# Performance work log

Measured on AMD Instinct MI355X. Metric: run time of the kernel, lower is better.

Reference implementation:

```python
import jax, jax.numpy as jnp
import numpy as np

N = 50000        # nodes
E = 1_600_000    # edges
F_IN = 128
HID = 128
OUT = 128
NEG_SLOPE = 0.2  # PyG GATConv default


def _gat_layer(x, src, dst, W, a_src, a_dst, b, n_nodes):
    """PyG GATConv (heads=1, add_self_loops handled by caller)."""
    h = x @ W                                   # [N, d_out]
    alpha_src = h @ a_src                       # [N]
    alpha_dst = h @ a_dst                       # [N]
    e = jax.nn.leaky_relu(alpha_src[src] + alpha_dst[dst], NEG_SLOPE)  # [E']
    # segment softmax over incoming edges of each destination node
    m = jax.ops.segment_max(e, dst, num_segments=n_nodes)
    e = jnp.exp(e - m[dst])
    s = jax.ops.segment_sum(e, dst, num_segments=n_nodes)
    alpha = e / s[dst]                          # [E']
    out = jax.ops.segment_sum(alpha[:, None] * h[src], dst, num_segments=n_nodes)
    return out + b


def setup_inputs() -> dict:
    key = jax.random.key(0)
    ks = jax.random.split(key, 11)
    sW1 = 1.0 / np.sqrt(F_IN)
    sW2 = 1.0 / np.sqrt(HID)
    return {
        "x": jax.random.normal(ks[0], (N, F_IN), dtype=jnp.float32),
        "edge_index": jax.random.randint(ks[1], (2, E), 0, N, dtype=jnp.int64
                                         if jax.config.jax_enable_x64 else jnp.int32),
        "W1": jax.random.normal(ks[2], (F_IN, HID), dtype=jnp.float32) * sW1,
        "a1_src": jax.random.normal(ks[3], (HID,), dtype=jnp.float32) * sW2,
        "a1_dst": jax.random.normal(ks[4], (HID,), dtype=jnp.float32) * sW2,
        "b1": jnp.zeros((HID,), dtype=jnp.float32),
        "W2": jax.random.normal(ks[5], (HID, OUT), dtype=jnp.float32) * sW2,
        "a2_src": jax.random.normal(ks[6], (OUT,), dtype=jnp.float32) * sW2,
        "a2_dst": jax.random.normal(ks[7], (OUT,), dtype=jnp.float32) * sW2,
        "b2": jnp.zeros((OUT,), dtype=jnp.float32),
    }


def reference(x, edge_index, W1, a1_src, a1_dst, b1, W2, a2_src, a2_dst, b2):
    n = x.shape[0]
    loop = jnp.arange(n, dtype=edge_index.dtype)
    src = jnp.concatenate([edge_index[0], loop])   # add self loops (PyG default)
    dst = jnp.concatenate([edge_index[1], loop])
    h = _gat_layer(x, src, dst, W1, a1_src, a1_dst, b1, n)
    h = jax.nn.relu(h)
    # F.dropout with training=False is identity (eval-mode reference)
    out = _gat_layer(h, src, dst, W2, a2_src, a2_dst, b2, n)
    return out
```

## Files before the change

kernel.cpp:

```cpp
#include <hip/hip_runtime.h>
#include <hip/hip_bf16.h>
#include <hip/hip_fp16.h>

#define FD 128
#define CBW 256
#define NBK 256

typedef _Float16 half8 __attribute__((ext_vector_type(8)));
typedef float f32x4 __attribute__((ext_vector_type(4)));

__global__ __launch_bounds__(256) void k_pre(const int* __restrict__ dst,
                                             int* __restrict__ ccnt, int e, int nb,
                                             const float* __restrict__ W1,
                                             const float* __restrict__ W2,
                                             __half* __restrict__ T1,
                                             __half* __restrict__ T2) {
    __shared__ float sw[128 * 129];
    const int t = threadIdx.x;
    if (blockIdx.x < 256) {
        int* lh = (int*)sw;
        if (t < NBK) lh[t] = 0;
        __syncthreads();
        for (int i = blockIdx.x * 256 + t; i < e; i += 256 * 256)
            atomicAdd(&lh[dst[i] >> 8], 1);
        __syncthreads();
        if (t < nb) {
            int c = lh[t];
            if (c) atomicAdd(&ccnt[t], c);
        }
    } else {
        const float* W = (blockIdx.x == 257) ? W2 : W1;
        __half* T = (blockIdx.x == 257) ? T2 : T1;
#pragma unroll
        for (int i = 0; i < 64; i++) {
            int idx = i * 256 + t;
            sw[(idx >> 7) * 129 + (idx & 127)] = W[idx];
        }
        __syncthreads();
#pragma unroll
        for (int i = 0; i < 32; i++) {
            int o = i * 256 + t;
            int c = o >> 6, kp = o & 63;
            float lo = sw[(kp * 2) * 129 + c];
            float hi = sw[(kp * 2 + 1) * 129 + c];
            *(__half2*)&T[c * 128 + kp * 2] = __floats2half2_rn(lo, hi);
        }
    }
}

__global__ void k_cscan(const int* __restrict__ ccnt, int* __restrict__ cbase,
                        int* __restrict__ ccur, int nb, int* __restrict__ rowptr, int n) {
    __shared__ int wsum[16];
    __shared__ int woff[17];
    const int t = threadIdx.x, lane = t & 63, wid = t >> 6;
    int v = (t < nb) ? ccnt[t] : 0;
    int s = v;
#pragma unroll
    for (int off = 1; off < 64; off <<= 1) {
        int u = __shfl_up(s, off, 64);
        if (lane >= off) s += u;
    }
    if (lane == 63) wsum[wid] = s;
    __syncthreads();
    if (wid == 0) {
        int w2 = (lane < 16) ? wsum[lane] : 0;
#pragma unroll
        for (int off = 1; off < 16; off <<= 1) {
            int u = __shfl_up(w2, off, 64);
            if (lane >= off) w2 += u;
        }
        if (lane < 16) woff[lane + 1] = w2;
        if (lane == 0) woff[0] = 0;
    }
    __syncthreads();
    int excl = woff[wid] + (s - v);
    if (t < nb) { cbase[t] = excl; ccur[t] = excl; }
    if (t == 0) { cbase[nb] = woff[16]; rowptr[n] = woff[16]; }
}

__global__ __launch_bounds__(256) void k_mid(const int* __restrict__ src,
                                             const int* __restrict__ dst,
                                             int* __restrict__ ccur,
                                             int* __restrict__ ebuf,
                                             int e, int nb, int nscat,
                                             const float* __restrict__ X,
                                             const __half* __restrict__ Wt,
                                             const float* __restrict__ a_s,
                                             const float* __restrict__ a_d,
                                             __half* __restrict__ H,
                                             float* __restrict__ as_,
                                             float* __restrict__ ad_, int n) {
    __shared__ int lh[NBK];
    __shared__ int lb[NBK];
    const int t = threadIdx.x;
    if ((int)blockIdx.x < nscat) {
        const int per = (e + nscat - 1) / nscat;
        const int lo = blockIdx.x * per;
        const int hi = min(e, lo + per);
        if (t < NBK) lh[t] = 0;
        __syncthreads();
        for (int i = lo + t; i < hi; i += 256) atomicAdd(&lh[dst[i] >> 8], 1);
        __syncthreads();
        if (t < nb) {
            int c = lh[t];
            lb[t] = c ? atomicAdd(&ccur[t], c) : 0;
        }
        __syncthreads();
        if (t < NBK) lh[t] = 0;
        __syncthreads();
        for (int i = lo + t; i < hi; i += 256) {
            int d = dst[i];
            int bkt = d >> 8;
            int r = atomicAdd(&lh[bkt], 1);
            ebuf[lb[bkt] + r] = (src[i] << 8) | (d & (CBW - 1));
        }
    } else {
        const int bid = blockIdx.x - nscat;
        const int wave = t >> 6, lane = t & 63;
        const int g = lane >> 4, c16 = lane & 15;
        const int row0 = bid * 64 + wave * 16;

        half8 A[4];
        {
            int row = row0 + c16;
            int rc = (row < n) ? row : (n - 1);
            const float* xp = &X[(size_t)rc * 128 + g * 8];
#pragma unroll
            for (int kc = 0; kc < 4; kc++) {
                float4 x0 = *(const float4*)(xp + kc * 32);
                float4 x1 = *(const float4*)(xp + kc * 32 + 4);
                half8 a;
                a[0] = (_Float16)x0.x; a[1] = (_Float16)x0.y;
                a[2] = (_Float16)x0.z; a[3] = (_Float16)x0.w;
                a[4] = (_Float16)x1.x; a[5] = (_Float16)x1.y;
                a[6] = (_Float16)x1.z; a[7] = (_Float16)x1.w;
                A[kc] = a;
            }
        }
        f32x4 acc[8];
#pragma unroll
        for (int ct = 0; ct < 8; ct++) acc[ct] = (f32x4){0.f, 0.f, 0.f, 0.f};
#pragma unroll
        for (int ct = 0; ct < 8; ct++) {
            const __half* wp = &Wt[(ct * 16 + c16) * 128 + g * 8];
#pragma unroll
            for (int kc = 0; kc < 4; kc++) {
                half8 b = *(const half8*)(wp + kc * 32);
                acc[ct] = __builtin_amdgcn_mfma_f32_16x16x32_f16(A[kc], b, acc[ct], 0, 0, 0);
            }
        }
        float asv[8], adv[8];
#pragma unroll
        for (int ct = 0; ct < 8; ct++) {
            asv[ct] = a_s[ct * 16 + c16];
            adv[ct] = a_d[ct * 16 + c16];
        }
#pragma unroll
        for (int r = 0; r < 4; r++) {
            const int row = row0 + g * 4 + r;
            float vs = 0.f, vd = 0.f;
#pragma unroll
            for (int ct = 0; ct < 8; ct++) {
                float v = acc[ct][r];
                vs += v * asv[ct];
                vd += v * adv[ct];
                if (row < n) H[(size_t)row * 128 + ct * 16 + c16] = __float2half(v);
            }
#pragma unroll
            for (int off = 8; off; off >>= 1) {
                vs += __shfl_xor(vs, off, 16);
                vd += __shfl_xor(vd, off, 16);
            }
            if (c16 == 0 && row < n) { as_[row] = vs; ad_[row] = vd; }
        }
    }
}

__global__ __launch_bounds__(256) void k_fine(const int* __restrict__ ebuf,
                                              const int* __restrict__ cbase,
                                              int* __restrict__ rowptr,
                                              int* __restrict__ colidx, int n) {
    const int b = blockIdx.x;
    const int node0 = b * CBW;
    const int nloc = min(CBW, n - node0);
    const int beg = cbase[b], end = cbase[b + 1];
    __shared__ int fh[CBW];
    __shared__ int fo[CBW];
    __shared__ int wt4[4];
    const int t = threadIdx.x, lane = t & 63, wid = t >> 6;
    fh[t] = 0;
    __syncthreads();
    for (int e = beg + t; e < end; e += 256) atomicAdd(&fh[ebuf[e] & (CBW - 1)], 1);
    __syncthreads();
    {
        int v = fh[t];
        int s = v;
#pragma unroll
        for (int off = 1; off < 64; off <<= 1) {
            int u = __shfl_up(s, off, 64);
            if (lane >= off) s += u;
        }
        if (lane == 63) wt4[wid] = s;
        __syncthreads();
        int wo = 0;
#pragma unroll
        for (int j = 0; j < 4; j++) wo += (j < wid) ? wt4[j] : 0;
        fo[t] = wo + s - v;
    }
    __syncthreads();
    if (t < nloc) rowptr[node0 + t] = beg + fo[t];
    fh[t] = 0;
    __syncthreads();
    for (int e = beg + t; e < end; e += 256) {
        int v = ebuf[e];
        int d = v & (CBW - 1);
        int r = atomicAdd(&fh[d], 1);
        colidx[beg + fo[d] + r] = v >> 8;
    }
}

__global__ __launch_bounds__(256) void k_gemm(const __half* __restrict__ X,
                                              const __half* __restrict__ Wt,
                                              const float* __restrict__ a_s,
                                              const float* __restrict__ a_d,
                                              __half* __restrict__ H,
                                              float* __restrict__ as_,
                                              float* __restrict__ ad_, int n) {
    const int t = threadIdx.x;
    const int wave = t >> 6, lane = t & 63;
    const int g = lane >> 4, c16 = lane & 15;
    const int row0 = blockIdx.x * 64 + wave * 16;

    half8 A[4];
    {
        int row = row0 + c16;
        int rc = (row < n) ? row : (n - 1);
        const __half* xp = &X[(size_t)rc * 128 + g * 8];
#pragma unroll
        for (int kc = 0; kc < 4; kc++) A[kc] = *(const half8*)(xp + kc * 32);
    }
    f32x4 acc[8];
#pragma unroll
    for (int ct = 0; ct < 8; ct++) acc[ct] = (f32x4){0.f, 0.f, 0.f, 0.f};
#pragma unroll
    for (int ct = 0; ct < 8; ct++) {
        const __half* wp = &Wt[(ct * 16 + c16) * 128 + g * 8];
#pragma unroll
        for (int kc = 0; kc < 4; kc++) {
            half8 b = *(const half8*)(wp + kc * 32);
            acc[ct] = __builtin_amdgcn_mfma_f32_16x16x32_f16(A[kc], b, acc[ct], 0, 0, 0);
        }
    }
    float asv[8], adv[8];
#pragma unroll
    for (int ct = 0; ct < 8; ct++) {
        asv[ct] = a_s[ct * 16 + c16];
        adv[ct] = a_d[ct * 16 + c16];
    }
#pragma unroll
    for (int r = 0; r < 4; r++) {
        const int row = row0 + g * 4 + r;
        float vs = 0.f, vd = 0.f;
#pragma unroll
        for (int ct = 0; ct < 8; ct++) {
            float v = acc[ct][r];
            vs += v * asv[ct];
            vd += v * adv[ct];
            if (row < n) H[(size_t)row * 128 + ct * 16 + c16] = __float2half(v);
        }
#pragma unroll
        for (int off = 8; off; off >>= 1) {
            vs += __shfl_xor(vs, off, 16);
            vd += __shfl_xor(vd, off, 16);
        }
        if (c16 == 0 && row < n) { as_[row] = vs; ad_[row] = vd; }
    }
}

__device__ __forceinline__ void fmix8(float* acc, uint4 hv, float w) {
    union { uint4 u; _Float16 h[8]; } c;
    c.u = hv;
#pragma unroll
    for (int j = 0; j < 8; j++) acc[j] += w * (float)c.h[j];
}

__global__ __launch_bounds__(256) void k_aggr(const __half* __restrict__ H,
                                              const float* __restrict__ as_,
                                              const float* __restrict__ ad_,
                                              const int* __restrict__ rowptr,
                                              const int* __restrict__ colidx,
                                              const float* __restrict__ bias,
                                              float* __restrict__ outf,
                                              __half* __restrict__ outh,
                                              int n, int mode) {
    __shared__ int2 pr[4][64];
    const int wid = threadIdx.x >> 6;
    const int lane = threadIdx.x & 63;
    const int node = blockIdx.x * 4 + wid;
    if (node >= n) return;
    const int q = lane >> 4;
    const int boff = (lane & 15) * 16;
    const char* Hb = (const char*)H + boff;
    const float adn = ad_[node];
    float sp = 0.f;
    float acc[8] = {0.f, 0.f, 0.f, 0.f, 0.f, 0.f, 0.f, 0.f};
    const int beg = rowptr[node], end = rowptr[node + 1];

    {
        float e = as_[node] + adn;
        e = (e > 0.f) ? e : 0.2f * e;
        const float w = __expf(e);
        if (lane == 63) sp += w;
        if (q == 3) {
            const uint4 hv = *(const uint4*)(Hb + ((unsigned)node << 8));
            fmix8(acc, hv, w);
        }
    }

    for (int it = beg; it < end; it += 64) {
        const int idx = it + lane;
        const bool valid = idx < end;
        const int sl = colidx[valid ? idx : (end - 1)];
        float e = as_[sl] + adn;
        e = (e > 0.f) ? e : 0.2f * e;
        const float w = valid ? __expf(e) : 0.f;
        sp += w;
        pr[wid][lane] = make_int2((int)((unsigned)sl << 8), __float_as_int(w));
        int m = end - it; if (m > 64) m = 64;
        const int iters = (m + 3) >> 2;
        int slot = q;
#pragma unroll 4
        for (int g = 0; g < iters; ++g) {
            const int2 p = pr[wid][slot];
            const float wg = __int_as_float(p.y);
            const uint4 hv = *(const uint4*)(Hb + (unsigned)p.x);
            fmix8(acc, hv, wg);
            slot += 4;
        }
    }

#pragma unroll
    for (int off = 1; off < 64; off <<= 1) sp += __shfl_xor(sp, off);
#pragma unroll
    for (int off = 16; off <= 32; off <<= 1) {
#pragma unroll
        for (int j = 0; j < 8; j++) acc[j] += __shfl_xor(acc[j], off);
    }
    if (q == 0) {
        const int f0 = boff >> 1;
        const float inv = 1.f / sp;
        float o[8];
        const float4 b0 = *(const float4*)&bias[f0];
        const float4 b1 = *(const float4*)&bias[f0 + 4];
        o[0] = acc[0] * inv + b0.x; o[1] = acc[1] * inv + b0.y;
        o[2] = acc[2] * inv + b0.z; o[3] = acc[3] * inv + b0.w;
        o[4] = acc[4] * inv + b1.x; o[5] = acc[5] * inv + b1.y;
        o[6] = acc[6] * inv + b1.z; o[7] = acc[7] * inv + b1.w;
        if (mode == 1) {
#pragma unroll
            for (int j = 0; j < 8; j++) o[j] = fmaxf(o[j], 0.f);
            union { __half2 h2[4]; uint4 u; } pkk;
            pkk.h2[0] = __floats2half2_rn(o[0], o[1]);
            pkk.h2[1] = __floats2half2_rn(o[2], o[3]);
            pkk.h2[2] = __floats2half2_rn(o[4], o[5]);
            pkk.h2[3] = __floats2half2_rn(o[6], o[7]);
            *(uint4*)&outh[(size_t)node * 128 + f0] = pkk.u;
        } else {
            *(float4*)&outf[(size_t)node * 128 + f0] = make_float4(o[0], o[1], o[2], o[3]);
            *(float4*)&outf[(size_t)node * 128 + f0 + 4] = make_float4(o[4], o[5], o[6], o[7]);
        }
    }
}

extern "C" void kernel_launch(void* const* d_in, const int* in_sizes, int n_in,
                              void* d_out, int out_size, void* d_ws, size_t ws_size,
                              hipStream_t stream) {
    const float* x   = (const float*)d_in[0];
    const int*   ei  = (const int*)d_in[1];
    const float* W1  = (const float*)d_in[2];
    const float* a1s = (const float*)d_in[3];
    const float* a1d = (const float*)d_in[4];
    const float* b1  = (const float*)d_in[5];
    const float* W2  = (const float*)d_in[6];
    const float* a2s = (const float*)d_in[7];
    const float* a2d = (const float*)d_in[8];
    const float* b2  = (const float*)d_in[9];
    float* dout = (float*)d_out;

    const int n = in_sizes[0] / FD;
    const int E = in_sizes[1] / 2;
    const int* src = ei;
    const int* dst = ei + E;
    const int NB = (n + CBW - 1) / CBW;

    char* base = (char*)d_ws;
    __half* buf0  = (__half*)base;
    int*    ebuf  = (int*)base;
    __half* H     = (__half*)(base + (size_t)n * FD * sizeof(__half));
    float* as_    = (float*)((char*)H + (size_t)n * FD * sizeof(__half));
    float* ad_    = as_ + n;
    int*   rowptr = (int*)(ad_ + n);
    int*   ccnt   = rowptr + (n + 1);
    int*   cbase  = ccnt + NB;
    int*   ccur   = cbase + NB + 1;
    int*   colidx = ccur + NB;
    size_t wt_off = (((size_t)((char*)(colidx + E) - base)) + 15) & ~(size_t)15;
    __half* Wt1h  = (__half*)(base + wt_off);
    __half* Wt2h  = Wt1h + 128 * 128;

    const int gemm_grid = (n + 63) / 64;
    const int node_grid = (n + 3) / 4;
    const int SCAT = 256;

    hipMemsetAsync(ccnt, 0, (size_t)NB * sizeof(int), stream);
    k_pre<<<258, 256, 0, stream>>>(dst, ccnt, E, NB, W1, W2, Wt1h, Wt2h);
    k_cscan<<<1, 1024, 0, stream>>>(ccnt, cbase, ccur, NB, rowptr, n);
    k_mid<<<SCAT + gemm_grid, 256, 0, stream>>>(src, dst, ccur, ebuf, E, NB, SCAT,
                                                x, Wt1h, a1s, a1d, H, as_, ad_, n);
    k_fine<<<NB, 256, 0, stream>>>(ebuf, cbase, rowptr, colidx, n);
    k_aggr<<<node_grid, 256, 0, stream>>>(H, as_, ad_, rowptr, colidx, b1,
                                          nullptr, buf0, n, 1);
    k_gemm<<<gemm_grid, 256, 0, stream>>>(buf0, Wt2h, a2s, a2d, H, as_, ad_, n);
    k_aggr<<<node_grid, 256, 0, stream>>>(H, as_, ad_, rowptr, colidx, b2,
                                          dout, nullptr, n, 0);
}
```

Baseline: 219.2 us.

## Shrink CSR buckets to 128 nodes and regroup gemm with histogram kernel

Bucket width for the two-level CSR build drops from 256 to 128 nodes, giving up to 512 coarse buckets, which adds parallelism in k_fine. The layer-1 GEMM now co-launches with the coarse histogram instead of the scatter, and the scatter runs as its own kernel. The memset is folded into the weight-transpose kernel, which now runs first. The scan and scatter still depend on NB fitting the 1024-thread scan, and the new split means one more dependent launch.

```diff
diff --git a/kernel.cpp b/kernel.cpp
--- a/kernel.cpp
+++ b/kernel.cpp
@@ -3,119 +3,64 @@
 #include <hip/hip_fp16.h>
 
 #define FD 128
-#define CBW 256
-#define NBK 256
+#define CBW 128
+#define NBK 512
 
 typedef _Float16 half8 __attribute__((ext_vector_type(8)));
 typedef float f32x4 __attribute__((ext_vector_type(4)));
 
-__global__ __launch_bounds__(256) void k_pre(const int* __restrict__ dst,
-                                             int* __restrict__ ccnt, int e, int nb,
-                                             const float* __restrict__ W1,
-                                             const float* __restrict__ W2,
-                                             __half* __restrict__ T1,
-                                             __half* __restrict__ T2) {
+__global__ __launch_bounds__(256) void k_wz(const float* __restrict__ W1,
+                                            const float* __restrict__ W2,
+                                            __half* __restrict__ T1,
+                                            __half* __restrict__ T2,
+                                            int* __restrict__ ccnt, int nb) {
+    const int t = threadIdx.x;
+    if (blockIdx.x == 2) {
+        for (int i = t; i < nb; i += 256) ccnt[i] = 0;
+        return;
+    }
     __shared__ float sw[128 * 129];
+    const float* W = blockIdx.x ? W2 : W1;
+    __half* T = blockIdx.x ? T2 : T1;
+#pragma unroll
+    for (int i = 0; i < 64; i++) {
+        int idx = i * 256 + t;
+        sw[(idx >> 7) * 129 + (idx & 127)] = W[idx];
+    }
+    __syncthreads();
+#pragma unroll
+    for (int i = 0; i < 32; i++) {
+        int o = i * 256 + t;
+        int c = o >> 6, kp = o & 63;
+        float lo = sw[(kp * 2) * 129 + c];
+        float hi = sw[(kp * 2 + 1) * 129 + c];
+        *(__half2*)&T[c * 128 + kp * 2] = __floats2half2_rn(lo, hi);
+    }
+}
+
+__global__ __launch_bounds__(256) void k_pg(const int* __restrict__ dst,
+                                            int* __restrict__ ccnt, int e, int nb,
+                                            const float* __restrict__ X,
+                                            const __half* __restrict__ Wt,
+                                            const float* __restrict__ a_s,
+                                            const float* __restrict__ a_d,
+                                            __half* __restrict__ H,
+                                            float* __restrict__ as_,
+                                            float* __restrict__ ad_, int n) {
+    __shared__ int lh[NBK];
     const int t = threadIdx.x;
     if (blockIdx.x < 256) {
-        int* lh = (int*)sw;
-        if (t < NBK) lh[t] = 0;
+        for (int i = t; i < NBK; i += 256) lh[i] = 0;
         __syncthreads();
         for (int i = blockIdx.x * 256 + t; i < e; i += 256 * 256)
-            atomicAdd(&lh[dst[i] >> 8], 1);
+            atomicAdd(&lh[dst[i] >> 7], 1);
         __syncthreads();
-        if (t < nb) {
-            int c = lh[t];
-            if (c) atomicAdd(&ccnt[t], c);
+        for (int i = t; i < nb; i += 256) {
+            int c = lh[i];
+            if (c) atomicAdd(&ccnt[i], c);
         }
     } else {
-        const float* W = (blockIdx.x == 257) ? W2 : W1;
-        __half* T = (blockIdx.x == 257) ? T2 : T1;
-#pragma unroll
-        for (int i = 0; i < 64; i++) {
-            int idx = i * 256 + t;
-            sw[(idx >> 7) * 129 + (idx & 127)] = W[idx];
-        }
-        __syncthreads();
-#pragma unroll
-        for (int i = 0; i < 32; i++) {
-            int o = i * 256 + t;
-            int c = o >> 6, kp = o & 63;
-            float lo = sw[(kp * 2) * 129 + c];
-            float hi = sw[(kp * 2 + 1) * 129 + c];
-            *(__half2*)&T[c * 128 + kp * 2] = __floats2half2_rn(lo, hi);
-        }
-    }
-}
-
-__global__ void k_cscan(const int* __restrict__ ccnt, int* __restrict__ cbase,
-                        int* __restrict__ ccur, int nb, int* __restrict__ rowptr, int n) {
-    __shared__ int wsum[16];
-    __shared__ int woff[17];
-    const int t = threadIdx.x, lane = t & 63, wid = t >> 6;
-    int v = (t < nb) ? ccnt[t] : 0;
-    int s = v;
-#pragma unroll
-    for (int off = 1; off < 64; off <<= 1) {
-        int u = __shfl_up(s, off, 64);
-        if (lane >= off) s += u;
-    }
-    if (lane == 63) wsum[wid] = s;
-    __syncthreads();
-    if (wid == 0) {
-        int w2 = (lane < 16) ? wsum[lane] : 0;
-#pragma unroll
-        for (int off = 1; off < 16; off <<= 1) {
-            int u = __shfl_up(w2, off, 64);
-            if (lane >= off) w2 += u;
-        }
-        if (lane < 16) woff[lane + 1] = w2;
-        if (lane == 0) woff[0] = 0;
-    }
-    __syncthreads();
-    int excl = woff[wid] + (s - v);
-    if (t < nb) { cbase[t] = excl; ccur[t] = excl; }
-    if (t == 0) { cbase[nb] = woff[16]; rowptr[n] = woff[16]; }
-}
-
-__global__ __launch_bounds__(256) void k_mid(const int* __restrict__ src,
-                                             const int* __restrict__ dst,
-                                             int* __restrict__ ccur,
-                                             int* __restrict__ ebuf,
-                                             int e, int nb, int nscat,
-                                             const float* __restrict__ X,
-                                             const __half* __restrict__ Wt,
-                                             const float* __restrict__ a_s,
-                                             const float* __restrict__ a_d,
-                                             __half* __restrict__ H,
-                                             float* __restrict__ as_,
-                                             float* __restrict__ ad_, int n) {
-    __shared__ int lh[NBK];
-    __shared__ int lb[NBK];
-    const int t = threadIdx.x;
-    if ((int)blockIdx.x < nscat) {
-        const int per = (e + nscat - 1) / nscat;
-        const int lo = blockIdx.x * per;
-        const int hi = min(e, lo + per);
-        if (t < NBK) lh[t] = 0;
-        __syncthreads();
-        for (int i = lo + t; i < hi; i += 256) atomicAdd(&lh[dst[i] >> 8], 1);
-        __syncthreads();
-        if (t < nb) {
-            int c = lh[t];
-            lb[t] = c ? atomicAdd(&ccur[t], c) : 0;
-        }
-        __syncthreads();
-        if (t < NBK) lh[t] = 0;
-        __syncthreads();
-        for (int i = lo + t; i < hi; i += 256) {
-            int d = dst[i];
-            int bkt = d >> 8;
-            int r = atomicAdd(&lh[bkt], 1);
-            ebuf[lb[bkt] + r] = (src[i] << 8) | (d & (CBW - 1));
-        }
-    } else {
-        const int bid = blockIdx.x - nscat;
+        const int bid = blockIdx.x - 256;
         const int wave = t >> 6, lane = t & 63;
         const int g = lane >> 4, c16 = lane & 15;
         const int row0 = bid * 64 + wave * 16;
@@ -176,6 +121,66 @@
     }
 }
 
+__global__ void k_cscan(const int* __restrict__ ccnt, int* __restrict__ cbase,
+                        int* __restrict__ ccur, int nb, int* __restrict__ rowptr, int n) {
+    __shared__ int wsum[16];
+    __shared__ int woff[17];
+    const int t = threadIdx.x, lane = t & 63, wid = t >> 6;
+    int v = (t < nb) ? ccnt[t] : 0;
+    int s = v;
+#pragma unroll
+    for (int off = 1; off < 64; off <<= 1) {
+        int u = __shfl_up(s, off, 64);
+        if (lane >= off) s += u;
+    }
+    if (lane == 63) wsum[wid] = s;
+    __syncthreads();
+    if (wid == 0) {
+        int w2 = (lane < 16) ? wsum[lane] : 0;
+#pragma unroll
+        for (int off = 1; off < 16; off <<= 1) {
+            int u = __shfl_up(w2, off, 64);
+            if (lane >= off) w2 += u;
+        }
+        if (lane < 16) woff[lane + 1] = w2;
+        if (lane == 0) woff[0] = 0;
+    }
+    __syncthreads();
+    int excl = woff[wid] + (s - v);
+    if (t < nb) { cbase[t] = excl; ccur[t] = excl; }
+    if (t == 0) { cbase[nb] = woff[16]; rowptr[n] = woff[16]; }
+}
+
+__global__ __launch_bounds__(256) void k_scat(const int* __restrict__ src,
+                                              const int* __restrict__ dst,
+                                              int* __restrict__ ccur,
+                                              int* __restrict__ ebuf,
+                                              int e, int nb, int nscat) {
+    __shared__ int lh[NBK];
+    __shared__ int lb[NBK];
+    const int t = threadIdx.x;
+    const int per = (e + nscat - 1) / nscat;
+    const int lo = blockIdx.x * per;
+    const int hi = min(e, lo + per);
+    for (int i = t; i < NBK; i += 256) lh[i] = 0;
+    __syncthreads();
+    for (int i = lo + t; i < hi; i += 256) atomicAdd(&lh[dst[i] >> 7], 1);
+    __syncthreads();
+    for (int i = t; i < nb; i += 256) {
+        int c = lh[i];
+        lb[i] = c ? atomicAdd(&ccur[i], c) : 0;
+    }
+    __syncthreads();
+    for (int i = t; i < NBK; i += 256) lh[i] = 0;
+    __syncthreads();
+    for (int i = lo + t; i < hi; i += 256) {
+        int d = dst[i];
+        int bkt = d >> 7;
+        int r = atomicAdd(&lh[bkt], 1);
+        ebuf[lb[bkt] + r] = (src[i] << 7) | (d & (CBW - 1));
+    }
+}
+
 __global__ __launch_bounds__(256) void k_fine(const int* __restrict__ ebuf,
                                               const int* __restrict__ cbase,
                                               int* __restrict__ rowptr,
@@ -186,36 +191,34 @@
     const int beg = cbase[b], end = cbase[b + 1];
     __shared__ int fh[CBW];
     __shared__ int fo[CBW];
-    __shared__ int wt4[4];
-    const int t = threadIdx.x, lane = t & 63, wid = t >> 6;
-    fh[t] = 0;
+    __shared__ int w0tot;
+    const int t = threadIdx.x;
+    if (t < CBW) fh[t] = 0;
     __syncthreads();
     for (int e = beg + t; e < end; e += 256) atomicAdd(&fh[ebuf[e] & (CBW - 1)], 1);
     __syncthreads();
-    {
-        int v = fh[t];
-        int s = v;
+    int v = 0, s = 0;
+    if (t < CBW) {
+        v = fh[t];
+        s = v;
 #pragma unroll
         for (int off = 1; off < 64; off <<= 1) {
             int u = __shfl_up(s, off, 64);
-            if (lane >= off) s += u;
-        }
-        if (lane == 63) wt4[wid] = s;
-        __syncthreads();
-        int wo = 0;
-#pragma unroll
-        for (int j = 0; j < 4; j++) wo += (j < wid) ? wt4[j] : 0;
-        fo[t] = wo + s - v;
-    }
+            if ((t & 63) >= off) s += u;
+        }
+        if (t == 63) w0tot = s;
+    }
+    __syncthreads();
+    if (t < CBW) fo[t] = ((t >= 64) ? w0tot : 0) + s - v;
     __syncthreads();
     if (t < nloc) rowptr[node0 + t] = beg + fo[t];
-    fh[t] = 0;
+    if (t < CBW) fh[t] = 0;
     __syncthreads();
     for (int e = beg + t; e < end; e += 256) {
-        int v = ebuf[e];
-        int d = v & (CBW - 1);
+        int rec = ebuf[e];
+        int d = rec & (CBW - 1);
         int r = atomicAdd(&fh[d], 1);
-        colidx[beg + fo[d] + r] = v >> 8;
+        colidx[beg + fo[d] + r] = rec >> 7;
     }
 }
 
@@ -412,11 +415,11 @@
     const int node_grid = (n + 3) / 4;
     const int SCAT = 256;
 
-    hipMemsetAsync(ccnt, 0, (size_t)NB * sizeof(int), stream);
-    k_pre<<<258, 256, 0, stream>>>(dst, ccnt, E, NB, W1, W2, Wt1h, Wt2h);
+    k_wz<<<3, 256, 0, stream>>>(W1, W2, Wt1h, Wt2h, ccnt, NB);
+    k_pg<<<256 + gemm_grid, 256, 0, stream>>>(dst, ccnt, E, NB,
+                                              x, Wt1h, a1s, a1d, H, as_, ad_, n);
     k_cscan<<<1, 1024, 0, stream>>>(ccnt, cbase, ccur, NB, rowptr, n);
-    k_mid<<<SCAT + gemm_grid, 256, 0, stream>>>(src, dst, ccur, ebuf, E, NB, SCAT,
-                                                x, Wt1h, a1s, a1d, H, as_, ad_, n);
+    k_scat<<<SCAT, 256, 0, stream>>>(src, dst, ccur, ebuf, E, NB, SCAT);
     k_fine<<<NB, 256, 0, stream>>>(ebuf, cbase, rowptr, colidx, n);
     k_aggr<<<node_grid, 256, 0, stream>>>(H, as_, ad_, rowptr, colidx, b1,
                                           nullptr, buf0, n, 1);
```

Result: faster. 208.4 us (-4.9%).
